# Kernel optimization log

Measured on AMD Instinct MI355X. Metric: run time of the kernel, lower is better.

Reference implementation:

```python
import jax, jax.numpy as jnp
import numpy as np

NUM_GRIDS = 16
IN_X, IN_Z, OUT, BATCH = 32, 32, 64, 512


def _borders_cdf_grid(n_chunks):
    def inv_cdf(u):
        return np.log(2.0 * u) if u <= 0.5 else -np.log(2.0 * (1.0 - u))
    cs = 1.0 / n_chunks
    b = [inv_cdf(i * cs) for i in range(1, n_chunks)]
    left = b[0] - (b[1] - b[0])
    right = b[-1] + (b[-1] - b[-2])
    return np.array([left] + b + [right], dtype=np.float32)


def _laplace_cdf(v):
    e = jnp.exp(-jnp.abs(v))
    return jnp.where(v > 0, 1.0 - 0.5 * e, 0.5 * e)


def setup_inputs() -> dict:
    key = jax.random.key(0)
    k1, k2, k3 = jax.random.split(key, 3)
    scale = 0.1 / np.sqrt(IN_X * IN_Z)
    borders_np = _borders_cdf_grid(NUM_GRIDS)
    inv_len_np = (1.0 / (borders_np[1:] - borders_np[:-1])).astype(np.float32)
    return {
        "x": jax.random.normal(k1, (IN_X, BATCH), dtype=jnp.float32),
        "z": jax.random.normal(k2, (IN_Z, BATCH), dtype=jnp.float32),
        "func_parameter": jax.random.uniform(
            k3, (NUM_GRIDS + 1, NUM_GRIDS + 1, OUT, IN_X, IN_Z),
            dtype=jnp.float32, minval=-scale, maxval=scale),
        "borders": jnp.asarray(borders_np),
        "inverse_chunk_lengths": jnp.asarray(inv_len_np[:NUM_GRIDS]),
    }


def reference(x, z, func_parameter, borders, inverse_chunk_lengths):
    G = inverse_chunk_lengths.shape[0]
    Ix, B = x.shape
    Iz = z.shape[0]

    # data-dependent bin indices per (input_dim, batch) element
    idx_x = jnp.clip((_laplace_cdf(x) * G).astype(jnp.int32), 0, G - 1)  # [Ix,B]
    idx_z = jnp.clip((_laplace_cdf(z) * G).astype(jnp.int32), 0, G - 1)  # [Iz,B]
    dx = (x - borders[idx_x]) * inverse_chunk_lengths[idx_x]             # [Ix,B]
    dz = (z - borders[idx_z]) * inverse_chunk_lengths[idx_z]             # [Iz,B]
    idx_xn = jnp.clip(idx_x + 1, 0, G)
    idx_zn = jnp.clip(idx_z + 1, 0, G)

    # [Ix, Iz, G+1, G+1, O] so the per-(ix,iz) tables are leading-indexed
    Pt = jnp.transpose(func_parameter, (3, 4, 0, 1, 2))
    ax = jnp.arange(Ix)[:, None, None]   # [Ix,1,1]
    az = jnp.arange(Iz)[None, :, None]   # [1,Iz,1]

    def corner(ii, jj):  # ii:[Ix,1,B] or broadcastable, jj:[1,Iz,B]
        return Pt[ax, az, ii, jj]        # -> [Ix,Iz,B,O]

    ixb, ixnb = idx_x[:, None, :], idx_xn[:, None, :]
    izb, iznb = idx_z[None, :, :], idx_zn[None, :, :]
    wx, wz = dx[:, None, :], dz[None, :, :]             # [Ix,1,B],[1,Iz,B]

    out = (
        jnp.einsum('xzb,xzbo->ob', (1 - wx) * (1 - wz), corner(ixb, izb))
        + jnp.einsum('xzb,xzbo->ob', (1 - wx) * wz, corner(ixb, iznb))
        + jnp.einsum('xzb,xzbo->ob', wx * (1 - wz), corner(ixnb, izb))
        + jnp.einsum('xzb,xzbo->ob', wx * wz, corner(ixnb, iznb))
    )
    return out  # [output_dim, batch]
```

## Files before the change

kernel.cpp:

```cpp
#include <hip/hip_runtime.h>


#define NG        16
#define NB        17
#define IN_X      32
#define IN_Z      32
#define OUT_DIM   64
#define BATCH     512
#define CELLS     (NB * NB)
#define LDS_STR   33
#define XSTR      (NB * LDS_STR)
#define QT        (CELLS * 8)
#define NITER     5

__device__ __forceinline__ void grid_coord(float v,
                                           const float* __restrict__ borders,
                                           const float* __restrict__ inv_len,
                                           int& idx, float& w) {
    float e   = expf(-fabsf(v));
    float cdf = (v > 0.f) ? (1.f - 0.5f * e) : (0.5f * e);
    int t = (int)(cdf * 16.f);
    t = t < 0 ? 0 : (t > NG - 1 ? NG - 1 : t);
    idx = t;
    w = (v - borders[t]) * inv_len[t];
}

__device__ __forceinline__ unsigned pack_bf16(float a, float b) {
    unsigned ua = __float_as_uint(a);
    unsigned ub = __float_as_uint(b);
    ua += 0x7FFFu + ((ua >> 16) & 1u);
    ub += 0x7FFFu + ((ub >> 16) & 1u);
    return (ua >> 16) | (ub & 0xFFFF0000u);
}
__device__ __forceinline__ float bf_lo(unsigned u) {
    return __uint_as_float(u << 16);
}
__device__ __forceinline__ float bf_hi(unsigned u) {
    return __uint_as_float(u & 0xFFFF0000u);
}

__global__ void precompute_kernel(const float* __restrict__ x,
                                  const float* __restrict__ z,
                                  const float* __restrict__ borders,
                                  const float* __restrict__ inv_len,
                                  float2* __restrict__ xc,
                                  uint2* __restrict__ zc2,
                                  float* __restrict__ out) {
    const int gid = blockIdx.x * blockDim.x + threadIdx.x;
    out[gid] = 0.f;
    int idx; float w;
    if (gid < IN_X * BATCH) {
        grid_coord(x[gid], borders, inv_len, idx, w);
        xc[gid] = make_float2(w, __int_as_float(idx * XSTR));
    } else {
        const int g = gid - IN_X * BATCH;
        const int j = g >> 9;
        const int b = g & (BATCH - 1);
        grid_coord(z[g], borders, inv_len, idx, w);
        zc2[b * IN_Z + j] = make_uint2(__float_as_uint(w),
                                       (unsigned)(idx * LDS_STR));
    }
}

__global__ __launch_bounds__(512, 8)
void bf2d_kernel(const float2* __restrict__ xc,
                 const uint2* __restrict__ zc2,
                 const float* __restrict__ P,
                 float* __restrict__ out) {
    __shared__ unsigned lds[CELLS * LDS_STR];

    const int tid = threadIdx.x;
    const int o0  = (blockIdx.x & 31) * 2;
    const int i   = blockIdx.x >> 5;

    const float* Pbase = P + (size_t)o0 * 1024 + (size_t)i * 32;
    #pragma unroll
    for (int t = 0; t < NITER; ++t) {
        const int k = tid + t * 512;
        if (k < QT) {
            const int c  = k >> 3;
            const int j4 = (k & 7) << 2;
            const float* g = Pbase + (size_t)c * 65536 + j4;
            const float4 a = *(const float4*)g;
            const float4 b = *(const float4*)(g + 1024);
            unsigned* d = &lds[c * LDS_STR + j4];
            d[0] = pack_bf16(a.x, b.x);
            d[1] = pack_bf16(a.y, b.y);
            d[2] = pack_bf16(a.z, b.z);
            d[3] = pack_bf16(a.w, b.w);
        }
    }
    __syncthreads();

    const float2 xcv  = xc[i * BATCH + tid];
    const float  wx   = xcv.x;
    const int    xoff = __float_as_int(xcv.y);

    const uint4* zp4 = (const uint4*)(zc2 + (size_t)tid * IN_Z);
    float accx = 0.f, accy = 0.f;
    #pragma unroll 4
    for (int jj = 0; jj < 16; ++jj) {
        const uint4 q = zp4[jj];
        {
            const float wz   = __uint_as_float(q.x);
            const int   base = xoff + (int)q.y + 2 * jj;
            const unsigned a0 = lds[base];
            const unsigned a1 = lds[base + LDS_STR];
            const unsigned b0 = lds[base + XSTR];
            const unsigned b1 = lds[base + XSTR + LDS_STR];
            const float lox = bf_lo(a0) + wz * (bf_lo(a1) - bf_lo(a0));
            const float loy = bf_hi(a0) + wz * (bf_hi(a1) - bf_hi(a0));
            const float hix = bf_lo(b0) + wz * (bf_lo(b1) - bf_lo(b0));
            const float hiy = bf_hi(b0) + wz * (bf_hi(b1) - bf_hi(b0));
            accx += lox + wx * (hix - lox);
            accy += loy + wx * (hiy - loy);
        }
        {
            const float wz   = __uint_as_float(q.z);
            const int   base = xoff + (int)q.w + 2 * jj + 1;
            const unsigned a0 = lds[base];
            const unsigned a1 = lds[base + LDS_STR];
            const unsigned b0 = lds[base + XSTR];
            const unsigned b1 = lds[base + XSTR + LDS_STR];
            const float lox = bf_lo(a0) + wz * (bf_lo(a1) - bf_lo(a0));
            const float loy = bf_hi(a0) + wz * (bf_hi(a1) - bf_hi(a0));
            const float hix = bf_lo(b0) + wz * (bf_lo(b1) - bf_lo(b0));
            const float hiy = bf_hi(b0) + wz * (bf_hi(b1) - bf_hi(b0));
            accx += lox + wx * (hix - lox);
            accy += loy + wx * (hiy - loy);
        }
    }

    atomicAdd(&out[o0 * BATCH + tid],       accx);
    atomicAdd(&out[(o0 + 1) * BATCH + tid], accy);
}

extern "C" void kernel_launch(void* const* d_in, const int* in_sizes, int n_in,
                              void* d_out, int out_size, void* d_ws, size_t ws_size,
                              hipStream_t stream) {
    const float* x       = (const float*)d_in[0];
    const float* z       = (const float*)d_in[1];
    const float* P       = (const float*)d_in[2];
    const float* borders = (const float*)d_in[3];
    const float* inv_len = (const float*)d_in[4];
    float* out = (float*)d_out;

    float2* xc  = (float2*)d_ws;
    uint2*  zc2 = (uint2*)(xc + IN_X * BATCH);

    precompute_kernel<<<dim3(128), dim3(256), 0, stream>>>(
        x, z, borders, inv_len, xc, zc2, out);

    bf2d_kernel<<<dim3((OUT_DIM / 2) * IN_X), dim3(512), 0, stream>>>(
        xc, zc2, P, out);
}
```

Measured before the change: 131.9 us.

## Add repack kernel converting parameters to contiguous bf16 tiles before main kernel

A new kernel reads the fp32 parameter tensor once, packs output pairs into bf16 words, and writes them into a layout where each (output-pair, input-x) block's table is contiguous. The main kernel then streams half the bytes with contiguous uint4 loads and no longer does conversion work during LDS staging. In exchange, an extra full pass over the parameters and a write of the packed copy is added on every call, which raises total memory traffic.

```diff
diff --git a/kernel.cpp b/kernel.cpp
--- a/kernel.cpp
+++ b/kernel.cpp
@@ -10,8 +10,9 @@
 #define CELLS     (NB * NB)
 #define LDS_STR   33
 #define XSTR      (NB * LDS_STR)
-#define QT        (CELLS * 8)
-#define NITER     5
+#define QROW      (CELLS * 32)
+#define SQT       (QROW / 4)
+#define SNITER    5
 
 __device__ __forceinline__ void grid_coord(float v,
                                            const float* __restrict__ borders,
@@ -62,32 +63,54 @@
     }
 }
 
+__global__ __launch_bounds__(256)
+void repack_kernel(const float* __restrict__ P,
+                   unsigned* __restrict__ Q) {
+    const int cell = blockIdx.x >> 2;
+    const int q    = blockIdx.x & 3;
+    const float* Pc = P + (size_t)cell * 65536;
+
+    #pragma unroll
+    for (int it = 0; it < 8; ++it) {
+        const int t   = threadIdx.x + it * 256;
+        const int opl = t >> 8;
+        const int rem = t & 255;
+        const int i   = rem >> 3;
+        const int j4  = (rem & 7) << 2;
+        const int op  = q * 8 + opl;
+
+        const float* g = Pc + (size_t)(2 * op) * 1024 + i * 32 + j4;
+        const float4 a = *(const float4*)g;
+        const float4 b = *(const float4*)(g + 1024);
+
+        unsigned* d = Q + (size_t)(op * 32 + i) * QROW + cell * 32 + j4;
+        *(uint4*)d = make_uint4(pack_bf16(a.x, b.x), pack_bf16(a.y, b.y),
+                                pack_bf16(a.z, b.z), pack_bf16(a.w, b.w));
+    }
+}
+
 __global__ __launch_bounds__(512, 8)
 void bf2d_kernel(const float2* __restrict__ xc,
                  const uint2* __restrict__ zc2,
-                 const float* __restrict__ P,
+                 const unsigned* __restrict__ Q,
                  float* __restrict__ out) {
     __shared__ unsigned lds[CELLS * LDS_STR];
 
     const int tid = threadIdx.x;
-    const int o0  = (blockIdx.x & 31) * 2;
+    const int op  = blockIdx.x & 31;
     const int i   = blockIdx.x >> 5;
+    const int o0  = op * 2;
 
-    const float* Pbase = P + (size_t)o0 * 1024 + (size_t)i * 32;
+    const uint4* Qb = (const uint4*)(Q + (size_t)(op * 32 + i) * QROW);
     #pragma unroll
-    for (int t = 0; t < NITER; ++t) {
+    for (int t = 0; t < SNITER; ++t) {
         const int k = tid + t * 512;
-        if (k < QT) {
+        if (k < SQT) {
             const int c  = k >> 3;
             const int j4 = (k & 7) << 2;
-            const float* g = Pbase + (size_t)c * 65536 + j4;
-            const float4 a = *(const float4*)g;
-            const float4 b = *(const float4*)(g + 1024);
+            const uint4 v = Qb[k];
             unsigned* d = &lds[c * LDS_STR + j4];
-            d[0] = pack_bf16(a.x, b.x);
-            d[1] = pack_bf16(a.y, b.y);
-            d[2] = pack_bf16(a.z, b.z);
-            d[3] = pack_bf16(a.w, b.w);
+            d[0] = v.x; d[1] = v.y; d[2] = v.z; d[3] = v.w;
         }
     }
     __syncthreads();
@@ -145,12 +168,15 @@
     const float* inv_len = (const float*)d_in[4];
     float* out = (float*)d_out;
 
-    float2* xc  = (float2*)d_ws;
-    uint2*  zc2 = (uint2*)(xc + IN_X * BATCH);
+    float2*   xc  = (float2*)d_ws;
+    uint2*    zc2 = (uint2*)(xc + IN_X * BATCH);
+    unsigned* Q   = (unsigned*)((char*)d_ws + 262144);
 
     precompute_kernel<<<dim3(128), dim3(256), 0, stream>>>(
         x, z, borders, inv_len, xc, zc2, out);
 
+    repack_kernel<<<dim3(CELLS * 4), dim3(256), 0, stream>>>(P, Q);
+
     bf2d_kernel<<<dim3((OUT_DIM / 2) * IN_X), dim3(512), 0, stream>>>(
-        xc, zc2, P, out);
+        xc, zc2, Q, out);
 }
```

New measurement: 144.7 us. 1.1x slower.
